# Kernel tuning notes

Measured on AMD Instinct MI355X. Metric: run time of the kernel, lower is better.

Reference implementation:

```python
import jax, jax.numpy as jnp
import numpy as np

N = 50000      # nodes
E = 800000     # edges
F_IN = 128     # input node feature dim
H = 4          # attention heads
DH = 64        # per-head hidden dim
HID = H * DH   # 256
NEG_SLOPE = 0.2


def gat_conv(h, src, dst, W, al, ar, b, res):
    # DGL GATConv: project, compute attention logits, edge softmax over dst, aggregate.
    feat = (h @ W).reshape(N, H, DH)                      # [N,H,DH]
    el = jnp.einsum('nhd,hd->nh', feat, al)               # [N,H]
    er = jnp.einsum('nhd,hd->nh', feat, ar)               # [N,H]
    e = el[src] + er[dst]                                 # [E,H]
    e = jnp.where(e > 0, e, NEG_SLOPE * e)                # LeakyReLU(0.2)
    m = jax.ops.segment_max(e, dst, num_segments=N)       # [N,H]
    m = jnp.where(jnp.isfinite(m), m, 0.0)                # zero-in-degree safety
    ex = jnp.exp(e - m[dst])                              # [E,H]
    denom = jax.ops.segment_sum(ex, dst, num_segments=N)  # [N,H]
    alpha = ex / jnp.maximum(denom[dst], 1e-16)           # edge softmax
    out = jax.ops.segment_sum(feat[src] * alpha[:, :, None], dst, num_segments=N)
    return out + res.reshape(N, H, DH) + b.reshape(1, H, DH)


def setup_inputs() -> dict:
    key = jax.random.key(0)
    ks = jax.random.split(key, 16)
    x = jax.random.normal(ks[0], (N, F_IN), jnp.float32)
    edge_index = jax.random.randint(ks[1], (2, E), 0, N)
    s_in = 1.0 / np.sqrt(F_IN)
    s_h = 1.0 / np.sqrt(HID)
    W0 = jax.random.normal(ks[2], (F_IN, HID), jnp.float32) * s_in
    W1 = jax.random.normal(ks[3], (HID, HID), jnp.float32) * s_h
    W2 = jax.random.normal(ks[4], (HID, HID), jnp.float32) * s_h
    al0 = jax.random.normal(ks[5], (H, DH), jnp.float32) * 0.1
    al1 = jax.random.normal(ks[6], (H, DH), jnp.float32) * 0.1
    al2 = jax.random.normal(ks[7], (H, DH), jnp.float32) * 0.1
    ar0 = jax.random.normal(ks[8], (H, DH), jnp.float32) * 0.1
    ar1 = jax.random.normal(ks[9], (H, DH), jnp.float32) * 0.1
    ar2 = jax.random.normal(ks[10], (H, DH), jnp.float32) * 0.1
    b0 = jnp.zeros((HID,), jnp.float32)
    b1 = jnp.zeros((HID,), jnp.float32)
    b2 = jnp.zeros((HID,), jnp.float32)
    resW0 = jax.random.normal(ks[11], (F_IN, HID), jnp.float32) * s_in
    return {"x": x, "edge_index": edge_index,
            "W0": W0, "W1": W1, "W2": W2,
            "al0": al0, "al1": al1, "al2": al2,
            "ar0": ar0, "ar1": ar1, "ar2": ar2,
            "b0": b0, "b1": b1, "b2": b2,
            "resW0": resW0}


def reference(x, edge_index, W0, W1, W2, al0, al1, al2, ar0, ar1, ar2, b0, b1, b2, resW0):
    src, dst = edge_index[0], edge_index[1]
    # layer 0: residual via linear projection (in != heads*hidden)
    h = gat_conv(x, src, dst, W0, al0, ar0, b0, x @ resW0).reshape(N, HID)
    h = jax.nn.relu(h)
    # layer 1: identity residual
    h = gat_conv(h, src, dst, W1, al1, ar1, b1, h).reshape(N, HID)
    h = jax.nn.relu(h)
    # layer 2: identity residual, mean over heads
    h = gat_conv(h, src, dst, W2, al2, ar2, b2, h)
    return h.mean(axis=1)  # [N, DH]
```

## Files before the change

kernel.cpp:

```cpp
#include <hip/hip_runtime.h>
#include <math.h>

#define N_NODES 50000
#define N_EDGES 800000
#define F_INPUT 128
#define HEADS 4
#define DHID 64
#define HID 256
#define M_PAD 50048
#define SCAN_B 49

typedef _Float16 half8 __attribute__((ext_vector_type(8)));
typedef _Float16 half4 __attribute__((ext_vector_type(4)));
typedef float f32x4 __attribute__((ext_vector_type(4)));


__global__ void hist_kernel(const int* __restrict__ dst, int* __restrict__ counts) {
    int e = blockIdx.x * 256 + threadIdx.x;
    if (e < N_EDGES) atomicAdd(&counts[dst[e]], 1);
}

__global__ __launch_bounds__(256) void scan1_kernel(const int* __restrict__ counts,
                                                    int* __restrict__ pre,
                                                    int* __restrict__ bsum) {
    __shared__ int buf[256];
    int tid = threadIdx.x;
    int idx = blockIdx.x * 1024 + tid * 4;
    int v0 = 0, v1 = 0, v2 = 0, v3 = 0;
    if (idx + 3 < N_NODES) {
        int4 v = *(const int4*)&counts[idx];
        v0 = v.x; v1 = v.y; v2 = v.z; v3 = v.w;
    } else {
        if (idx + 0 < N_NODES) v0 = counts[idx + 0];
        if (idx + 1 < N_NODES) v1 = counts[idx + 1];
        if (idx + 2 < N_NODES) v2 = counts[idx + 2];
    }
    int s0 = v0, s1 = s0 + v1, s2 = s1 + v2, s3 = s2 + v3;
    buf[tid] = s3;
    __syncthreads();
    for (int off = 1; off < 256; off <<= 1) {
        int t = (tid >= off) ? buf[tid - off] : 0;
        __syncthreads();
        buf[tid] += t;
        __syncthreads();
    }
    int excl = buf[tid] - s3;
    if (idx + 0 < N_NODES) pre[idx + 0] = excl + s0;
    if (idx + 1 < N_NODES) pre[idx + 1] = excl + s1;
    if (idx + 2 < N_NODES) pre[idx + 2] = excl + s2;
    if (idx + 3 < N_NODES) pre[idx + 3] = excl + s3;
    if (tid == 255) bsum[blockIdx.x] = buf[255];
}

__global__ void scan2_kernel(const int* __restrict__ bsum, int* __restrict__ bpre) {
    int lane = threadIdx.x;
    int v = (lane < SCAN_B) ? bsum[lane] : 0;
    int orig = v;
#pragma unroll
    for (int off = 1; off < 64; off <<= 1) {
        int t = __shfl_up(v, off, 64);
        if (lane >= off) v += t;
    }
    if (lane < SCAN_B) bpre[lane] = v - orig;
}

__global__ __launch_bounds__(256) void scan3_kernel(const int* __restrict__ pre,
                                                    const int* __restrict__ bpre,
                                                    int* __restrict__ row_ptr) {
    int add = bpre[blockIdx.x];
    int idx = blockIdx.x * 1024 + threadIdx.x * 4;
#pragma unroll
    for (int u = 0; u < 4; u++) {
        int i = idx + u;
        if (i < N_NODES) row_ptr[i + 1] = pre[i] + add;
    }
    if (blockIdx.x == 0 && threadIdx.x == 0) row_ptr[0] = 0;
}

__global__ void scatter_kernel(const int* __restrict__ src, const int* __restrict__ dst,
                               const int* __restrict__ row_ptr, int* __restrict__ cursor,
                               int* __restrict__ esrc) {
    int e = blockIdx.x * 256 + threadIdx.x;
    if (e < N_EDGES) {
        int d = dst[e];
        int pos = row_ptr[d] + atomicAdd(&cursor[d], 1);
        esrc[pos] = src[e];
    }
}


__global__ void cvt_x_kernel(const float* __restrict__ x, _Float16* __restrict__ x16) {
    int t = blockIdx.x * 256 + threadIdx.x;
    if (t < N_NODES * F_INPUT / 4) {
        f32x4 v = *(const f32x4*)&x[t * 4];
        half4 h = {(_Float16)v.x, (_Float16)v.y, (_Float16)v.z, (_Float16)v.w};
        *(half4*)&x16[(size_t)t * 4] = h;
    }
}

__global__ void wt_all_kernel(const float* __restrict__ W0, const float* __restrict__ WR,
                              _Float16* __restrict__ WtL0,
                              const float* __restrict__ W1, _Float16* __restrict__ Wt1,
                              const float* __restrict__ W2, _Float16* __restrict__ Wt2) {
    int t = blockIdx.x * 256 + threadIdx.x;
    if (t < 65536) {
        int c = t >> 7;
        int k = t & 127;
        float v = (c < 256) ? W0[k * 256 + c] : WR[k * 256 + (c - 256)];
        WtL0[t] = (_Float16)v;
    } else if (t < 131072) {
        int u = t - 65536;
        int c = u >> 8;
        int k = u & 255;
        Wt1[u] = (_Float16)W1[k * 256 + c];
    } else if (t < 196608) {
        int u = t - 131072;
        int c = u >> 8;
        int k = u & 255;
        Wt2[u] = (_Float16)W2[k * 256 + c];
    }
}

__global__ void wlwr_kernel(const float* __restrict__ W0, const float* __restrict__ al0,
                            const float* __restrict__ ar0, _Float16* __restrict__ WtL0,
                            const float* __restrict__ W1, const float* __restrict__ al1,
                            const float* __restrict__ ar1, _Float16* __restrict__ Wt1,
                            const float* __restrict__ W2, const float* __restrict__ al2,
                            const float* __restrict__ ar2, _Float16* __restrict__ Wt2) {
    int t = blockIdx.x * 256 + threadIdx.x;
    if (t < 2048) {
        int row8 = t >> 7, k = t & 127;
        float v = 0.f;
        if (row8 < 8) {
            int h = row8 & 3;
            const float* vec = (row8 < 4) ? al0 : ar0;
            float s = 0.f;
            for (int d = 0; d < 64; d++) s += W0[k * 256 + h * 64 + d] * vec[h * 64 + d];
            v = s;
        }
        WtL0[(512 + row8) * 128 + k] = (_Float16)v;
    } else if (t < 6144) {
        int u = t - 2048;
        int row8 = u >> 8, k = u & 255;
        float v = 0.f;
        if (row8 < 8) {
            int h = row8 & 3;
            const float* vec = (row8 < 4) ? al1 : ar1;
            float s = 0.f;
            for (int d = 0; d < 64; d++) s += W1[k * 256 + h * 64 + d] * vec[h * 64 + d];
            v = s;
        }
        Wt1[(256 + row8) * 256 + k] = (_Float16)v;
    } else if (t < 10240) {
        int u = t - 6144;
        int row8 = u >> 8, k = u & 255;
        float v = 0.f;
        if (row8 < 8) {
            int h = row8 & 3;
            const float* vec = (row8 < 4) ? al2 : ar2;
            float s = 0.f;
            for (int d = 0; d < 64; d++) s += W2[k * 256 + h * 64 + d] * vec[h * 64 + d];
            v = s;
        }
        Wt2[(256 + row8) * 256 + k] = (_Float16)v;
    }
}


__device__ __forceinline__ void gl2lds16(const void* g, void* l) {
    __builtin_amdgcn_global_load_lds((const __attribute__((address_space(1))) void*)g,
                                     (__attribute__((address_space(3))) void*)l, 16, 0, 0);
}

__global__ __launch_bounds__(512) void gemm_l0(const _Float16* __restrict__ A16,
                                               const _Float16* __restrict__ WtL0,
                                               _Float16* __restrict__ feat16,
                                               _Float16* __restrict__ res16,
                                               float* __restrict__ el, float* __restrict__ er) {
    __shared__ __align__(16) _Float16 As[4 * 512];
    __shared__ __align__(16) _Float16 Ws[33 * 512];
    int tid = threadIdx.x;
    int w = tid >> 6;
    int lane = tid & 63;
    int lrow = lane & 15;
    int lk = lane >> 4;
    int row0 = blockIdx.x * 64;

    f32x4 acc[4][4] = {};
    f32x4 acc5[4] = {};

    for (int k0 = 0; k0 < F_INPUT; k0 += 32) {
        if (w < 4)
            gl2lds16(A16 + (size_t)(row0 + w * 16 + lrow) * F_INPUT + k0 + lk * 8, &As[w * 512]);
#pragma unroll
        for (int i = 0; i < 4; i++) {
            int tt = i * 8 + w;
            gl2lds16(WtL0 + (size_t)(tt * 16 + lrow) * F_INPUT + k0 + lk * 8, &Ws[tt * 512]);
        }
        if (w == 7)
            gl2lds16(WtL0 + (size_t)(512 + lrow) * F_INPUT + k0 + lk * 8, &Ws[32 * 512]);
        __syncthreads();
        half8 a[4], b[4], b5;
#pragma unroll
        for (int m = 0; m < 4; m++) a[m] = *(const half8*)&As[m * 512 + lane * 8];
#pragma unroll
        for (int j = 0; j < 4; j++) b[j] = *(const half8*)&Ws[(w * 4 + j) * 512 + lane * 8];
        if (w == 3) b5 = *(const half8*)&Ws[32 * 512 + lane * 8];
#pragma unroll
        for (int m = 0; m < 4; m++)
#pragma unroll
            for (int j = 0; j < 4; j++)
                acc[m][j] = __builtin_amdgcn_mfma_f32_16x16x32_f16(a[m], b[j], acc[m][j], 0, 0, 0);
        if (w == 3) {
#pragma unroll
            for (int m = 0; m < 4; m++)
                acc5[m] = __builtin_amdgcn_mfma_f32_16x16x32_f16(a[m], b5, acc5[m], 0, 0, 0);
        }
        __syncthreads();
    }

    if (w < 4) {
#pragma unroll
        for (int m = 0; m < 4; m++) {
#pragma unroll
            for (int r = 0; r < 4; r++) {
                int row = row0 + m * 16 + lk * 4 + r;
                if (row < N_NODES) {
#pragma unroll
                    for (int j = 0; j < 4; j++)
                        feat16[(size_t)row * HID + w * 64 + j * 16 + lrow] = (_Float16)acc[m][j][r];
                }
            }
        }
        if (w == 3 && lrow < 8) {
#pragma unroll
            for (int m = 0; m < 4; m++) {
#pragma unroll
                for (int r = 0; r < 4; r++) {
                    int row = row0 + m * 16 + lk * 4 + r;
                    if (row < N_NODES) {
                        float v = acc5[m][r];
                        if (lrow < 4) el[row * 4 + lrow] = v;
                        else          er[row * 4 + (lrow - 4)] = v;
                    }
                }
            }
        }
    } else {
        int wc = w - 4;
#pragma unroll
        for (int m = 0; m < 4; m++) {
#pragma unroll
            for (int r = 0; r < 4; r++) {
                int row = row0 + m * 16 + lk * 4 + r;
                if (row < N_NODES) {
#pragma unroll
                    for (int j = 0; j < 4; j++)
                        res16[(size_t)row * HID + wc * 64 + j * 16 + lrow] = (_Float16)acc[m][j][r];
                }
            }
        }
    }
}

__global__ __launch_bounds__(512) void gemm_h(const _Float16* __restrict__ A16,
                                              const _Float16* __restrict__ Wt,
                                              _Float16* __restrict__ feat16,
                                              float* __restrict__ el, float* __restrict__ er) {
    __shared__ __align__(16) _Float16 As[8 * 512];
    __shared__ __align__(16) _Float16 Ws[17 * 512];
    int tid = threadIdx.x;
    int w = tid >> 6;
    int lane = tid & 63;
    int lrow = lane & 15;
    int lk = lane >> 4;
    int wrow = w >> 2;
    int wcol = w & 3;
    int row0 = blockIdx.x * 128;

    f32x4 acc[4][4] = {};
    f32x4 acc5[4] = {};

    for (int k0 = 0; k0 < HID; k0 += 32) {
        gl2lds16(A16 + (size_t)(row0 + w * 16 + lrow) * HID + k0 + lk * 8, &As[w * 512]);
        gl2lds16(Wt + (size_t)(w * 16 + lrow) * HID + k0 + lk * 8, &Ws[w * 512]);
        gl2lds16(Wt + (size_t)((w + 8) * 16 + lrow) * HID + k0 + lk * 8, &Ws[(w + 8) * 512]);
        if (w == 0)
            gl2lds16(Wt + (size_t)(256 + lrow) * HID + k0 + lk * 8, &Ws[16 * 512]);
        __syncthreads();
        half8 a[4], b[4], b5;
#pragma unroll
        for (int m = 0; m < 4; m++) a[m] = *(const half8*)&As[(wrow * 4 + m) * 512 + lane * 8];
#pragma unroll
        for (int j = 0; j < 4; j++) b[j] = *(const half8*)&Ws[(wcol * 4 + j) * 512 + lane * 8];
        if (wcol == 3) b5 = *(const half8*)&Ws[16 * 512 + lane * 8];
#pragma unroll
        for (int m = 0; m < 4; m++)
#pragma unroll
            for (int j = 0; j < 4; j++)
                acc[m][j] = __builtin_amdgcn_mfma_f32_16x16x32_f16(a[m], b[j], acc[m][j], 0, 0, 0);
        if (wcol == 3) {
#pragma unroll
            for (int m = 0; m < 4; m++)
                acc5[m] = __builtin_amdgcn_mfma_f32_16x16x32_f16(a[m], b5, acc5[m], 0, 0, 0);
        }
        __syncthreads();
    }

#pragma unroll
    for (int m = 0; m < 4; m++) {
#pragma unroll
        for (int r = 0; r < 4; r++) {
            int row = row0 + wrow * 64 + m * 16 + lk * 4 + r;
            if (row < N_NODES) {
#pragma unroll
                for (int j = 0; j < 4; j++)
                    feat16[(size_t)row * HID + wcol * 64 + j * 16 + lrow] = (_Float16)acc[m][j][r];
            }
        }
    }
    if (wcol == 3 && lrow < 8) {
#pragma unroll
        for (int m = 0; m < 4; m++) {
#pragma unroll
            for (int r = 0; r < 4; r++) {
                int row = row0 + wrow * 64 + m * 16 + lk * 4 + r;
                if (row < N_NODES) {
                    float v = acc5[m][r];
                    if (lrow < 4) el[row * 4 + lrow] = v;
                    else          er[row * 4 + (lrow - 4)] = v;
                }
            }
        }
    }
}


__global__ __launch_bounds__(256) void agg_kernel(const _Float16* __restrict__ feat16,
                                                  const float* __restrict__ el,
                                                  const float* __restrict__ er,
                                                  const int* __restrict__ row_ptr,
                                                  const int* __restrict__ esrc,
                                                  const _Float16* __restrict__ res16,
                                                  const float* __restrict__ bias,
                                                  _Float16* __restrict__ out16,
                                                  float* __restrict__ outmean,
                                                  int do_relu) {
    __shared__ float lds[4][64 * 5];
    int wv = threadIdx.x >> 6;
    int lane = threadIdx.x & 63;
    int n = blockIdx.x * 4 + wv;
    int head = lane >> 4;
    int start = row_ptr[n];
    int deg = row_ptr[n + 1] - start;
    f32x4 ern = *(const f32x4*)&er[n * 4];
    float* L = lds[wv];

    f32x4 acc = {0.f, 0.f, 0.f, 0.f};
    float smh = 0.f;

    if (deg <= 64) {
        int s = 0;
        f32x4 x = {-1e30f, -1e30f, -1e30f, -1e30f};
        if (lane < deg) {
            s = esrc[start + lane];
            f32x4 v = *(const f32x4*)&el[s * 4];
            v = v + ern;
            x.x = v.x > 0.f ? v.x : 0.2f * v.x;
            x.y = v.y > 0.f ? v.y : 0.2f * v.y;
            x.z = v.z > 0.f ? v.z : 0.2f * v.z;
            x.w = v.w > 0.f ? v.w : 0.2f * v.w;
        }
        f32x4 cm = x;
#pragma unroll
        for (int off = 1; off < 64; off <<= 1) {
            cm.x = fmaxf(cm.x, __shfl_xor(cm.x, off, 64));
            cm.y = fmaxf(cm.y, __shfl_xor(cm.y, off, 64));
            cm.z = fmaxf(cm.z, __shfl_xor(cm.z, off, 64));
            cm.w = fmaxf(cm.w, __shfl_xor(cm.w, off, 64));
        }
        f32x4 ex4;
        ex4.x = __expf(x.x - cm.x);
        ex4.y = __expf(x.y - cm.y);
        ex4.z = __expf(x.z - cm.z);
        ex4.w = __expf(x.w - cm.w);
        L[lane * 5 + 0] = ex4.x;
        L[lane * 5 + 1] = ex4.y;
        L[lane * 5 + 2] = ex4.z;
        L[lane * 5 + 3] = ex4.w;
        L[lane * 5 + 4] = __int_as_float(s);
        f32x4 cs = ex4;
#pragma unroll
        for (int off = 1; off < 64; off <<= 1) {
            cs.x += __shfl_xor(cs.x, off, 64);
            cs.y += __shfl_xor(cs.y, off, 64);
            cs.z += __shfl_xor(cs.z, off, 64);
            cs.w += __shfl_xor(cs.w, off, 64);
        }
        smh = (head == 0) ? cs.x : (head == 1) ? cs.y : (head == 2) ? cs.z : cs.w;

        int j = 0;
        for (; j + 4 <= deg; j += 4) {
            float exv[4]; int ssv[4];
#pragma unroll
            for (int u = 0; u < 4; u++) {
                exv[u] = L[(j + u) * 5 + head];
                ssv[u] = __float_as_int(L[(j + u) * 5 + 4]);
            }
            half4 f[4];
#pragma unroll
            for (int u = 0; u < 4; u++)
                f[u] = *(const half4*)&feat16[(size_t)ssv[u] * HID + lane * 4];
#pragma unroll
            for (int u = 0; u < 4; u++) {
                acc.x += exv[u] * (float)f[u].x;
                acc.y += exv[u] * (float)f[u].y;
                acc.z += exv[u] * (float)f[u].z;
                acc.w += exv[u] * (float)f[u].w;
            }
        }
        for (; j < deg; j++) {
            float ex = L[j * 5 + head];
            int ss = __float_as_int(L[j * 5 + 4]);
            half4 f = *(const half4*)&feat16[(size_t)ss * HID + lane * 4];
            acc.x += ex * (float)f.x;
            acc.y += ex * (float)f.y;
            acc.z += ex * (float)f.z;
            acc.w += ex * (float)f.w;
        }
    } else {
        f32x4 mx = {-1e30f, -1e30f, -1e30f, -1e30f};
        for (int base = 0; base < deg; base += 64) {
            int e = base + lane;
            int s = 0;
            f32x4 x = {-1e30f, -1e30f, -1e30f, -1e30f};
            if (e < deg) {
                s = esrc[start + e];
                f32x4 v = *(const f32x4*)&el[s * 4];
                v = v + ern;
                x.x = v.x > 0.f ? v.x : 0.2f * v.x;
                x.y = v.y > 0.f ? v.y : 0.2f * v.y;
                x.z = v.z > 0.f ? v.z : 0.2f * v.z;
                x.w = v.w > 0.f ? v.w : 0.2f * v.w;
            }
            f32x4 cm = x;
#pragma unroll
            for (int off = 1; off < 64; off <<= 1) {
                cm.x = fmaxf(cm.x, __shfl_xor(cm.x, off, 64));
                cm.y = fmaxf(cm.y, __shfl_xor(cm.y, off, 64));
                cm.z = fmaxf(cm.z, __shfl_xor(cm.z, off, 64));
                cm.w = fmaxf(cm.w, __shfl_xor(cm.w, off, 64));
            }
            f32x4 nmx;
            nmx.x = fmaxf(mx.x, cm.x);
            nmx.y = fmaxf(mx.y, cm.y);
            nmx.z = fmaxf(mx.z, cm.z);
            nmx.w = fmaxf(mx.w, cm.w);
            float mxh  = (head == 0) ? mx.x  : (head == 1) ? mx.y  : (head == 2) ? mx.z  : mx.w;
            float nmxh = (head == 0) ? nmx.x : (head == 1) ? nmx.y : (head == 2) ? nmx.z : nmx.w;
            float sc = __expf(mxh - nmxh);
            smh *= sc;
            acc = acc * sc;
            f32x4 ex4;
            ex4.x = __expf(x.x - nmx.x);
            ex4.y = __expf(x.y - nmx.y);
            ex4.z = __expf(x.z - nmx.z);
            ex4.w = __expf(x.w - nmx.w);
            L[lane * 5 + 0] = ex4.x;
            L[lane * 5 + 1] = ex4.y;
            L[lane * 5 + 2] = ex4.z;
            L[lane * 5 + 3] = ex4.w;
            L[lane * 5 + 4] = __int_as_float(s);
            f32x4 cs = ex4;
#pragma unroll
            for (int off = 1; off < 64; off <<= 1) {
                cs.x += __shfl_xor(cs.x, off, 64);
                cs.y += __shfl_xor(cs.y, off, 64);
                cs.z += __shfl_xor(cs.z, off, 64);
                cs.w += __shfl_xor(cs.w, off, 64);
            }
            smh += (head == 0) ? cs.x : (head == 1) ? cs.y : (head == 2) ? cs.z : cs.w;

            int cnt = min(64, deg - base);
            int j = 0;
            for (; j + 4 <= cnt; j += 4) {
                float exv[4]; int ssv[4];
#pragma unroll
                for (int u = 0; u < 4; u++) {
                    exv[u] = L[(j + u) * 5 + head];
                    ssv[u] = __float_as_int(L[(j + u) * 5 + 4]);
                }
                half4 f[4];
#pragma unroll
                for (int u = 0; u < 4; u++)
                    f[u] = *(const half4*)&feat16[(size_t)ssv[u] * HID + lane * 4];
#pragma unroll
                for (int u = 0; u < 4; u++) {
                    acc.x += exv[u] * (float)f[u].x;
                    acc.y += exv[u] * (float)f[u].y;
                    acc.z += exv[u] * (float)f[u].z;
                    acc.w += exv[u] * (float)f[u].w;
                }
            }
            for (; j < cnt; j++) {
                float ex = L[j * 5 + head];
                int ss = __float_as_int(L[j * 5 + 4]);
                half4 f = *(const half4*)&feat16[(size_t)ss * HID + lane * 4];
                acc.x += ex * (float)f.x;
                acc.y += ex * (float)f.y;
                acc.z += ex * (float)f.z;
                acc.w += ex * (float)f.w;
            }
            mx = nmx;
        }
    }

    float inv = 1.f / fmaxf(smh, 1e-16f);
    f32x4 o = acc * inv;
    half4 rv = *(const half4*)&res16[(size_t)n * HID + lane * 4];
    f32x4 bv = *(const f32x4*)&bias[lane * 4];
    o.x += (float)rv.x + bv.x;
    o.y += (float)rv.y + bv.y;
    o.z += (float)rv.z + bv.z;
    o.w += (float)rv.w + bv.w;
    if (do_relu) {
        o.x = fmaxf(o.x, 0.f);
        o.y = fmaxf(o.y, 0.f);
        o.z = fmaxf(o.z, 0.f);
        o.w = fmaxf(o.w, 0.f);
    }
    if (outmean) {
        o.x += __shfl_xor(o.x, 16, 64); o.x += __shfl_xor(o.x, 32, 64);
        o.y += __shfl_xor(o.y, 16, 64); o.y += __shfl_xor(o.y, 32, 64);
        o.z += __shfl_xor(o.z, 16, 64); o.z += __shfl_xor(o.z, 32, 64);
        o.w += __shfl_xor(o.w, 16, 64); o.w += __shfl_xor(o.w, 32, 64);
        if (head == 0) {
            f32x4 mo = o * 0.25f;
            *(f32x4*)&outmean[(size_t)n * DHID + (lane & 15) * 4] = mo;
        }
    } else {
        half4 h = {(_Float16)o.x, (_Float16)o.y, (_Float16)o.z, (_Float16)o.w};
        *(half4*)&out16[(size_t)n * HID + lane * 4] = h;
    }
}


extern "C" void kernel_launch(void* const* d_in, const int* in_sizes, int n_in,
                              void* d_out, int out_size, void* d_ws, size_t ws_size,
                              hipStream_t stream) {
    const float* x     = (const float*)d_in[0];
    const int*   ei    = (const int*)d_in[1];
    const float* W0    = (const float*)d_in[2];
    const float* W1    = (const float*)d_in[3];
    const float* W2    = (const float*)d_in[4];
    const float* al0   = (const float*)d_in[5];
    const float* al1   = (const float*)d_in[6];
    const float* al2   = (const float*)d_in[7];
    const float* ar0   = (const float*)d_in[8];
    const float* ar1   = (const float*)d_in[9];
    const float* ar2   = (const float*)d_in[10];
    const float* b0    = (const float*)d_in[11];
    const float* b1    = (const float*)d_in[12];
    const float* b2    = (const float*)d_in[13];
    const float* resW0 = (const float*)d_in[14];
    float* out = (float*)d_out;

    const int* srcp = ei;
    const int* dstp = ei + N_EDGES;

    char* p = (char*)d_ws;
    auto alloc = [&](size_t bytes) -> char* {
        char* r = p;
        p += (bytes + 255) & ~(size_t)255;
        return r;
    };
    _Float16*  h16    = (_Float16*)alloc((size_t)M_PAD * HID * 2);
    _Float16*  feat16 = (_Float16*)alloc((size_t)M_PAD * HID * 2);
    _Float16*  res0   = (_Float16*)alloc((size_t)N_NODES * HID * 2);
    _Float16*  x16    = (_Float16*)alloc((size_t)M_PAD * F_INPUT * 2);
    float*     el     = (float*)alloc((size_t)N_NODES * HEADS * 4);
    float*     er     = (float*)alloc((size_t)N_NODES * HEADS * 4);
    _Float16*  WtL0   = (_Float16*)alloc((size_t)528 * F_INPUT * 2);
    _Float16*  Wt1    = (_Float16*)alloc((size_t)272 * HID * 2);
    _Float16*  Wt2    = (_Float16*)alloc((size_t)272 * HID * 2);
    int*       counts = (int*)alloc((size_t)2 * N_NODES * 4);
    int*       cursor = counts + N_NODES;
    int*       rowptr = (int*)alloc((size_t)(N_NODES + 1) * 4);
    int*       esrc   = (int*)alloc((size_t)N_EDGES * 4);
    int*       pre    = (int*)alloc((size_t)N_NODES * 4);
    int*       bsum   = (int*)alloc((size_t)SCAN_B * 4);
    int*       bpre   = (int*)alloc((size_t)SCAN_B * 4);

    const int EB = (N_EDGES + 255) / 256;
    const int NB = N_NODES / 4;

    hipMemsetAsync(counts, 0, (size_t)2 * N_NODES * 4, stream);
    hist_kernel<<<EB, 256, 0, stream>>>(dstp, counts);
    scan1_kernel<<<SCAN_B, 256, 0, stream>>>(counts, pre, bsum);
    scan2_kernel<<<1, 64, 0, stream>>>(bsum, bpre);
    scan3_kernel<<<SCAN_B, 256, 0, stream>>>(pre, bpre, rowptr);
    scatter_kernel<<<EB, 256, 0, stream>>>(srcp, dstp, rowptr, cursor, esrc);

    cvt_x_kernel<<<(N_NODES * F_INPUT / 4 + 255) / 256, 256, 0, stream>>>(x, x16);
    wt_all_kernel<<<768, 256, 0, stream>>>(W0, resW0, WtL0, W1, Wt1, W2, Wt2);
    wlwr_kernel<<<40, 256, 0, stream>>>(W0, al0, ar0, WtL0, W1, al1, ar1, Wt1, W2, al2, ar2, Wt2);

    gemm_l0<<<M_PAD / 64, 512, 0, stream>>>(x16, WtL0, feat16, res0, el, er);
    agg_kernel<<<NB, 256, 0, stream>>>(feat16, el, er, rowptr, esrc, res0, b0, h16, nullptr, 1);

    gemm_h<<<M_PAD / 128, 512, 0, stream>>>(h16, Wt1, feat16, el, er);
    agg_kernel<<<NB, 256, 0, stream>>>(feat16, el, er, rowptr, esrc, h16, b1, h16, nullptr, 1);

    gemm_h<<<M_PAD / 128, 512, 0, stream>>>(h16, Wt2, feat16, el, er);
    agg_kernel<<<NB, 256, 0, stream>>>(feat16, el, er, rowptr, esrc, h16, b2, nullptr, out, 0);
}
```

Baseline: 494.3 us.

## Degree-sort nodes for aggregation and drop softmax max pass

Three small kernels build a degree histogram, scan it, and produce a node order grouped by in-degree, so each 4-wave block of agg_kernel handles nodes of similar degree. The aggregation kernel is collapsed into a single chunked loop that skips the max-subtraction and its cross-lane max reduction and rescaling. It moves the sum reduction to the end, stores exp values per head in a padded LDS layout with precomputed byte offsets, and unrolls the gather by 8. The aim is to remove load imbalance between waves and the shuffle and exp overhead per edge chunk. In exchange, three extra tiny launches run in preprocessing, and unnormalized exp can overflow if attention logits become large.

After: 753.4 us. 1.52x slower.

```diff
diff --git a/kernel.cpp b/kernel.cpp
--- a/kernel.cpp
+++ b/kernel.cpp
@@ -9,6 +9,7 @@
 #define HID 256
 #define M_PAD 50048
 #define SCAN_B 49
+#define DMAX 128
 
 typedef _Float16 half8 __attribute__((ext_vector_type(8)));
 typedef _Float16 half4 __attribute__((ext_vector_type(4)));
@@ -85,6 +86,40 @@
         int d = dst[e];
         int pos = row_ptr[d] + atomicAdd(&cursor[d], 1);
         esrc[pos] = src[e];
+    }
+}
+
+
+__global__ void dhist_kernel(const int* __restrict__ counts, int* __restrict__ dhist) {
+    int t = blockIdx.x * 256 + threadIdx.x;
+    if (t < N_NODES) {
+        int d = min(counts[t], DMAX - 1);
+        atomicAdd(&dhist[d], 1);
+    }
+}
+
+__global__ void dscan_kernel(const int* __restrict__ dhist, int* __restrict__ dpre) {
+    __shared__ int buf[DMAX];
+    int tid = threadIdx.x;
+    int v = dhist[tid];
+    buf[tid] = v;
+    __syncthreads();
+    for (int off = 1; off < DMAX; off <<= 1) {
+        int t = (tid >= off) ? buf[tid - off] : 0;
+        __syncthreads();
+        buf[tid] += t;
+        __syncthreads();
+    }
+    dpre[tid] = buf[tid] - v;
+}
+
+__global__ void dorder_kernel(const int* __restrict__ counts, const int* __restrict__ dpre,
+                              int* __restrict__ dcur, int* __restrict__ norder) {
+    int t = blockIdx.x * 256 + threadIdx.x;
+    if (t < N_NODES) {
+        int d = min(counts[t], DMAX - 1);
+        int pos = dpre[d] + atomicAdd(&dcur[d], 1);
+        norder[pos] = t;
     }
 }
 
@@ -341,182 +376,86 @@
                                                   const float* __restrict__ er,
                                                   const int* __restrict__ row_ptr,
                                                   const int* __restrict__ esrc,
+                                                  const int* __restrict__ norder,
                                                   const _Float16* __restrict__ res16,
                                                   const float* __restrict__ bias,
                                                   _Float16* __restrict__ out16,
                                                   float* __restrict__ outmean,
                                                   int do_relu) {
-    __shared__ float lds[4][64 * 5];
+    __shared__ float lds[4][4 * 65 + 64];
     int wv = threadIdx.x >> 6;
     int lane = threadIdx.x & 63;
-    int n = blockIdx.x * 4 + wv;
+    int n = norder[blockIdx.x * 4 + wv];
     int head = lane >> 4;
     int start = row_ptr[n];
     int deg = row_ptr[n + 1] - start;
     f32x4 ern = *(const f32x4*)&er[n * 4];
     float* L = lds[wv];
+    float* Loff = L + 4 * 65;
+    const float* Lex = L + head * 65;
 
     f32x4 acc = {0.f, 0.f, 0.f, 0.f};
-    float smh = 0.f;
-
-    if (deg <= 64) {
-        int s = 0;
-        f32x4 x = {-1e30f, -1e30f, -1e30f, -1e30f};
-        if (lane < deg) {
-            s = esrc[start + lane];
+    f32x4 sm4 = {0.f, 0.f, 0.f, 0.f};
+    const char* fbase = (const char*)feat16 + lane * 8;
+
+    for (int base = 0; base < deg; base += 64) {
+        int e = base + lane;
+        f32x4 ex4 = {0.f, 0.f, 0.f, 0.f};
+        int off = 0;
+        if (e < deg) {
+            int s = esrc[start + e];
+            off = s * (HID * 2);
             f32x4 v = *(const f32x4*)&el[s * 4];
             v = v + ern;
-            x.x = v.x > 0.f ? v.x : 0.2f * v.x;
-            x.y = v.y > 0.f ? v.y : 0.2f * v.y;
-            x.z = v.z > 0.f ? v.z : 0.2f * v.z;
-            x.w = v.w > 0.f ? v.w : 0.2f * v.w;
-        }
-        f32x4 cm = x;
-#pragma unroll
-        for (int off = 1; off < 64; off <<= 1) {
-            cm.x = fmaxf(cm.x, __shfl_xor(cm.x, off, 64));
-            cm.y = fmaxf(cm.y, __shfl_xor(cm.y, off, 64));
-            cm.z = fmaxf(cm.z, __shfl_xor(cm.z, off, 64));
-            cm.w = fmaxf(cm.w, __shfl_xor(cm.w, off, 64));
-        }
-        f32x4 ex4;
-        ex4.x = __expf(x.x - cm.x);
-        ex4.y = __expf(x.y - cm.y);
-        ex4.z = __expf(x.z - cm.z);
-        ex4.w = __expf(x.w - cm.w);
-        L[lane * 5 + 0] = ex4.x;
-        L[lane * 5 + 1] = ex4.y;
-        L[lane * 5 + 2] = ex4.z;
-        L[lane * 5 + 3] = ex4.w;
-        L[lane * 5 + 4] = __int_as_float(s);
-        f32x4 cs = ex4;
-#pragma unroll
-        for (int off = 1; off < 64; off <<= 1) {
-            cs.x += __shfl_xor(cs.x, off, 64);
-            cs.y += __shfl_xor(cs.y, off, 64);
-            cs.z += __shfl_xor(cs.z, off, 64);
-            cs.w += __shfl_xor(cs.w, off, 64);
-        }
-        smh = (head == 0) ? cs.x : (head == 1) ? cs.y : (head == 2) ? cs.z : cs.w;
-
-        int j = 0;
-        for (; j + 4 <= deg; j += 4) {
-            float exv[4]; int ssv[4];
-#pragma unroll
-            for (int u = 0; u < 4; u++) {
-                exv[u] = L[(j + u) * 5 + head];
-                ssv[u] = __float_as_int(L[(j + u) * 5 + 4]);
-            }
-            half4 f[4];
-#pragma unroll
-            for (int u = 0; u < 4; u++)
-                f[u] = *(const half4*)&feat16[(size_t)ssv[u] * HID + lane * 4];
-#pragma unroll
-            for (int u = 0; u < 4; u++) {
-                acc.x += exv[u] * (float)f[u].x;
-                acc.y += exv[u] * (float)f[u].y;
-                acc.z += exv[u] * (float)f[u].z;
-                acc.w += exv[u] * (float)f[u].w;
-            }
-        }
-        for (; j < deg; j++) {
-            float ex = L[j * 5 + head];
-            int ss = __float_as_int(L[j * 5 + 4]);
-            half4 f = *(const half4*)&feat16[(size_t)ss * HID + lane * 4];
-            acc.x += ex * (float)f.x;
-            acc.y += ex * (float)f.y;
-            acc.z += ex * (float)f.z;
-            acc.w += ex * (float)f.w;
-        }
-    } else {
-        f32x4 mx = {-1e30f, -1e30f, -1e30f, -1e30f};
-        for (int base = 0; base < deg; base += 64) {
-            int e = base + lane;
-            int s = 0;
-            f32x4 x = {-1e30f, -1e30f, -1e30f, -1e30f};
-            if (e < deg) {
-                s = esrc[start + e];
-                f32x4 v = *(const f32x4*)&el[s * 4];
-                v = v + ern;
-                x.x = v.x > 0.f ? v.x : 0.2f * v.x;
-                x.y = v.y > 0.f ? v.y : 0.2f * v.y;
-                x.z = v.z > 0.f ? v.z : 0.2f * v.z;
-                x.w = v.w > 0.f ? v.w : 0.2f * v.w;
-            }
-            f32x4 cm = x;
-#pragma unroll
-            for (int off = 1; off < 64; off <<= 1) {
-                cm.x = fmaxf(cm.x, __shfl_xor(cm.x, off, 64));
-                cm.y = fmaxf(cm.y, __shfl_xor(cm.y, off, 64));
-                cm.z = fmaxf(cm.z, __shfl_xor(cm.z, off, 64));
-                cm.w = fmaxf(cm.w, __shfl_xor(cm.w, off, 64));
-            }
-            f32x4 nmx;
-            nmx.x = fmaxf(mx.x, cm.x);
-            nmx.y = fmaxf(mx.y, cm.y);
-            nmx.z = fmaxf(mx.z, cm.z);
-            nmx.w = fmaxf(mx.w, cm.w);
-            float mxh  = (head == 0) ? mx.x  : (head == 1) ? mx.y  : (head == 2) ? mx.z  : mx.w;
-            float nmxh = (head == 0) ? nmx.x : (head == 1) ? nmx.y : (head == 2) ? nmx.z : nmx.w;
-            float sc = __expf(mxh - nmxh);
-            smh *= sc;
-            acc = acc * sc;
-            f32x4 ex4;
-            ex4.x = __expf(x.x - nmx.x);
-            ex4.y = __expf(x.y - nmx.y);
-            ex4.z = __expf(x.z - nmx.z);
-            ex4.w = __expf(x.w - nmx.w);
-            L[lane * 5 + 0] = ex4.x;
-            L[lane * 5 + 1] = ex4.y;
-            L[lane * 5 + 2] = ex4.z;
-            L[lane * 5 + 3] = ex4.w;
-            L[lane * 5 + 4] = __int_as_float(s);
-            f32x4 cs = ex4;
-#pragma unroll
-            for (int off = 1; off < 64; off <<= 1) {
-                cs.x += __shfl_xor(cs.x, off, 64);
-                cs.y += __shfl_xor(cs.y, off, 64);
-                cs.z += __shfl_xor(cs.z, off, 64);
-                cs.w += __shfl_xor(cs.w, off, 64);
-            }
-            smh += (head == 0) ? cs.x : (head == 1) ? cs.y : (head == 2) ? cs.z : cs.w;
-
-            int cnt = min(64, deg - base);
-            int j = 0;
-            for (; j + 4 <= cnt; j += 4) {
-                float exv[4]; int ssv[4];
-#pragma unroll
-                for (int u = 0; u < 4; u++) {
-                    exv[u] = L[(j + u) * 5 + head];
-                    ssv[u] = __float_as_int(L[(j + u) * 5 + 4]);
-                }
-                half4 f[4];
-#pragma unroll
-                for (int u = 0; u < 4; u++)
-                    f[u] = *(const half4*)&feat16[(size_t)ssv[u] * HID + lane * 4];
-#pragma unroll
-                for (int u = 0; u < 4; u++) {
-                    acc.x += exv[u] * (float)f[u].x;
-                    acc.y += exv[u] * (float)f[u].y;
-                    acc.z += exv[u] * (float)f[u].z;
-                    acc.w += exv[u] * (float)f[u].w;
-                }
-            }
-            for (; j < cnt; j++) {
-                float ex = L[j * 5 + head];
-                int ss = __float_as_int(L[j * 5 + 4]);
-                half4 f = *(const half4*)&feat16[(size_t)ss * HID + lane * 4];
-                acc.x += ex * (float)f.x;
-                acc.y += ex * (float)f.y;
-                acc.z += ex * (float)f.z;
-                acc.w += ex * (float)f.w;
-            }
-            mx = nmx;
-        }
-    }
-
+            v.x = v.x > 0.f ? v.x : 0.2f * v.x;
+            v.y = v.y > 0.f ? v.y : 0.2f * v.y;
+            v.z = v.z > 0.f ? v.z : 0.2f * v.z;
+            v.w = v.w > 0.f ? v.w : 0.2f * v.w;
+            ex4.x = __expf(v.x);
+            ex4.y = __expf(v.y);
+            ex4.z = __expf(v.z);
+            ex4.w = __expf(v.w);
+        }
+        L[0 * 65 + lane] = ex4.x;
+        L[1 * 65 + lane] = ex4.y;
+        L[2 * 65 + lane] = ex4.z;
+        L[3 * 65 + lane] = ex4.w;
+        Loff[lane] = __int_as_float(off);
+        sm4 += ex4;
+
+        int cnt = min(64, deg - base);
+        int cnt8 = (cnt + 7) & ~7;
+        for (int j = 0; j < cnt8; j += 8) {
+            float ex[8]; int o[8];
+#pragma unroll
+            for (int u = 0; u < 8; u++) {
+                ex[u] = Lex[j + u];
+                o[u] = __float_as_int(Loff[j + u]);
+            }
+            half4 f[8];
+#pragma unroll
+            for (int u = 0; u < 8; u++) f[u] = *(const half4*)(fbase + o[u]);
+#pragma unroll
+            for (int u = 0; u < 8; u++) {
+                acc.x += ex[u] * (float)f[u].x;
+                acc.y += ex[u] * (float)f[u].y;
+                acc.z += ex[u] * (float)f[u].z;
+                acc.w += ex[u] * (float)f[u].w;
+            }
+        }
+    }
+
+#pragma unroll
+    for (int off2 = 1; off2 < 64; off2 <<= 1) {
+        sm4.x += __shfl_xor(sm4.x, off2, 64);
+        sm4.y += __shfl_xor(sm4.y, off2, 64);
+        sm4.z += __shfl_xor(sm4.z, off2, 64);
+        sm4.w += __shfl_xor(sm4.w, off2, 64);
+    }
+    float smh = (head == 0) ? sm4.x : (head == 1) ? sm4.y : (head == 2) ? sm4.z : sm4.w;
     float inv = 1.f / fmaxf(smh, 1e-16f);
     f32x4 o = acc * inv;
+
     half4 rv = *(const half4*)&res16[(size_t)n * HID + lane * 4];
     f32x4 bv = *(const f32x4*)&bias[lane * 4];
     o.x += (float)rv.x + bv.x;
@@ -583,34 +522,42 @@
     _Float16*  WtL0   = (_Float16*)alloc((size_t)528 * F_INPUT * 2);
     _Float16*  Wt1    = (_Float16*)alloc((size_t)272 * HID * 2);
     _Float16*  Wt2    = (_Float16*)alloc((size_t)272 * HID * 2);
-    int*       counts = (int*)alloc((size_t)2 * N_NODES * 4);
+    int*       counts = (int*)alloc(((size_t)2 * N_NODES + 2 * DMAX) * 4);
     int*       cursor = counts + N_NODES;
+    int*       dhist  = cursor + N_NODES;
+    int*       dcur   = dhist + DMAX;
     int*       rowptr = (int*)alloc((size_t)(N_NODES + 1) * 4);
     int*       esrc   = (int*)alloc((size_t)N_EDGES * 4);
     int*       pre    = (int*)alloc((size_t)N_NODES * 4);
     int*       bsum   = (int*)alloc((size_t)SCAN_B * 4);
     int*       bpre   = (int*)alloc((size_t)SCAN_B * 4);
+    int*       dpre   = (int*)alloc((size_t)DMAX * 4);
+    int*       norder = (int*)alloc((size_t)N_NODES * 4);
 
     const int EB = (N_EDGES + 255) / 256;
+    const int NBK = (N_NODES + 255) / 256;
     const int NB = N_NODES / 4;
 
-    hipMemsetAsync(counts, 0, (size_t)2 * N_NODES * 4, stream);
+    hipMemsetAsync(counts, 0, ((size_t)2 * N_NODES + 2 * DMAX) * 4, stream);
     hist_kernel<<<EB, 256, 0, stream>>>(dstp, counts);
     scan1_kernel<<<SCAN_B, 256, 0, stream>>>(counts, pre, bsum);
     scan2_kernel<<<1, 64, 0, stream>>>(bsum, bpre);
     scan3_kernel<<<SCAN_B, 256, 0, stream>>>(pre, bpre, rowptr);
     scatter_kernel<<<EB, 256, 0, stream>>>(srcp, dstp, rowptr, cursor, esrc);
+    dhist_kernel<<<NBK, 256, 0, stream>>>(counts, dhist);
+    dscan_kernel<<<1, DMAX, 0, stream>>>(dhist, dpre);
+    dorder_kernel<<<NBK, 256, 0, stream>>>(counts, dpre, dcur, norder);
 
     cvt_x_kernel<<<(N_NODES * F_INPUT / 4 + 255) / 256, 256, 0, stream>>>(x, x16);
     wt_all_kernel<<<768, 256, 0, stream>>>(W0, resW0, WtL0, W1, Wt1, W2, Wt2);
     wlwr_kernel<<<40, 256, 0, stream>>>(W0, al0, ar0, WtL0, W1, al1, ar1, Wt1, W2, al2, ar2, Wt2);
 
     gemm_l0<<<M_PAD / 64, 512, 0, stream>>>(x16, WtL0, feat16, res0, el, er);
-    agg_kernel<<<NB, 256, 0, stream>>>(feat16, el, er, rowptr, esrc, res0, b0, h16, nullptr, 1);
+    agg_kernel<<<NB, 256, 0, stream>>>(feat16, el, er, rowptr, esrc, norder, res0, b0, h16, nullptr, 1);
 
     gemm_h<<<M_PAD / 128, 512, 0, stream>>>(h16, Wt1, feat16, el, er);
-    agg_kernel<<<NB, 256, 0, stream>>>(feat16, el, er, rowptr, esrc, h16, b1, h16, nullptr, 1);
+    agg_kernel<<<NB, 256, 0, stream>>>(feat16, el, er, rowptr, esrc, norder, h16, b1, h16, nullptr, 1);
 
     gemm_h<<<M_PAD / 128, 512, 0, stream>>>(h16, Wt2, feat16, el, er);
-    agg_kernel<<<NB, 256, 0, stream>>>(feat16, el, er, rowptr, esrc, h16, b2, nullptr, out, 0);
-}
+    agg_kernel<<<NB, 256, 0, stream>>>(feat16, el, er, rowptr, esrc, norder, h16, b2, nullptr, out, 0);
+}
```
